# Optimization experiments

Measured on AMD Instinct MI355X. Metric: run time of the kernel, lower is better.

## Reference

```python
import jax, jax.numpy as jnp
import numpy as np

D_MODEL = 1024
NUM_HEADS = 16
HEAD_DIM = D_MODEL // NUM_HEADS
THETA = 10000.0
B, T = 2, 2048


def setup_inputs() -> dict:
    key = jax.random.key(0)
    k1, k2, k3 = jax.random.split(key, 3)
    x = jax.random.normal(k1, (B, T, D_MODEL), dtype=jnp.float32)
    W_qkv = jax.random.normal(k2, (3 * D_MODEL, D_MODEL), dtype=jnp.float32) * 0.02
    W_o = jax.random.normal(k3, (D_MODEL, D_MODEL), dtype=jnp.float32) * 0.02
    return {"x": x, "W_qkv": W_qkv, "W_o": W_o}


def _rope(x, cos, sin):
    # x: [B, h, T, d]; rotate interleaved even/odd pairs
    x_even = x[..., 0::2]
    x_odd = x[..., 1::2]
    out_even = x_even * cos - x_odd * sin
    out_odd = x_even * sin + x_odd * cos
    out = jnp.stack([out_even, out_odd], axis=-1)  # [B,h,T,d/2,2]
    return out.reshape(x.shape)


def reference(x, W_qkv, W_o):
    b, t, dm = x.shape
    # fused QKV projection (bias-free Linear: x @ W.T)
    qkv = jnp.einsum('btd,ed->bte', x, W_qkv)                # [B,T,3*D]
    qkv = qkv.reshape(b, t, 3, NUM_HEADS, HEAD_DIM)
    qkv = jnp.transpose(qkv, (2, 0, 3, 1, 4))                # [3,B,h,T,d]
    q, k, v = qkv[0], qkv[1], qkv[2]

    # RoPE with token_positions = arange(T)
    pos = jnp.arange(t, dtype=jnp.float32)                   # [T]
    inv_freq = THETA ** (-jnp.arange(0, HEAD_DIM, 2, dtype=jnp.float32) / HEAD_DIM)
    ang = pos[:, None] * inv_freq[None, :]                   # [T, d/2]
    cos = jnp.cos(ang)[None, None, :, :]
    sin = jnp.sin(ang)[None, None, :, :]
    q = _rope(q, cos, sin)
    k = _rope(k, cos, sin)

    # causal scaled dot-product attention
    scale = 1.0 / jnp.sqrt(jnp.asarray(HEAD_DIM, dtype=x.dtype))
    scores = jnp.einsum('bhqd,bhkd->bhqk', q, k) * scale     # [B,h,T,T]
    causal = jnp.tril(jnp.ones((t, t), dtype=bool))
    scores = jnp.where(causal[None, None, :, :], scores, -jnp.inf)
    attn = jax.nn.softmax(scores, axis=-1)
    out = jnp.einsum('bhqk,bhkd->bhqd', attn, v)             # [B,h,T,d]
    out = jnp.transpose(out, (0, 2, 1, 3)).reshape(b, t, dm) # [B,T,D]
    return jnp.einsum('btd,ed->bte', out, W_o)
```

## Files before the change

kernel.cpp:

```cpp
#include <hip/hip_runtime.h>
#include <hip/hip_bf16.h>
#include <cstdint>

#define NHEADS 16
#define HDIM 64
#define BB 2
#define TSEQ 2048
#define DM 1024
#define MROWS (BB*TSEQ)

typedef unsigned short u16;
typedef unsigned int u32;
typedef __bf16 bf16x8 __attribute__((ext_vector_type(8)));
typedef float f32x4 __attribute__((ext_vector_type(4)));

#define AS1C(p) ((const __attribute__((address_space(1))) u32*)(p))
#define AS3(p)  ((__attribute__((address_space(3))) u32*)(p))

static __device__ __forceinline__ u16 f2bf(float f) {
  return __builtin_bit_cast(u16, __float2bfloat16(f));
}
static __device__ __forceinline__ float bf2f(u16 u) {
  return __bfloat162float(__builtin_bit_cast(__hip_bfloat16, u));
}
static __device__ __forceinline__ u32 pack2bf(float a, float b) {
  const u32 ua = __builtin_bit_cast(u32, a) + 0x8000u;
  const u32 ub = __builtin_bit_cast(u32, b) + 0x8000u;
  return (ua >> 16) | (ub & 0xFFFF0000u);
}
static __device__ __forceinline__ f32x4 mfma16x16(bf16x8 a, bf16x8 b, f32x4 c) {
  return __builtin_amdgcn_mfma_f32_16x16x32_bf16(a, b, c, 0, 0, 0);
}

#define N4_X   (MROWS * DM / 4)
#define N4_WQ  (3 * DM * DM / 4)
#define N4_WO  (DM * DM / 4)
__global__ __launch_bounds__(256) void cast_all(const float* __restrict__ x,
                                                const float* __restrict__ wq,
                                                const float* __restrict__ wo,
                                                u16* __restrict__ xb,
                                                u16* __restrict__ wqb,
                                                u16* __restrict__ wob) {
  int i = blockIdx.x * 256 + threadIdx.x;
  const int stride = gridDim.x * 256;
  for (; i < N4_X + N4_WQ + N4_WO; i += stride) {
    const float4* src; u16* dst; int j;
    if (i < N4_X)            { src = (const float4*)x;  dst = xb;  j = i; }
    else if (i < N4_X + N4_WQ) { src = (const float4*)wq; dst = wqb; j = i - N4_X; }
    else                     { src = (const float4*)wo; dst = wob; j = i - N4_X - N4_WQ; }
    float4 v = src[j];
    ushort4 o;
    o.x = f2bf(v.x); o.y = f2bf(v.y); o.z = f2bf(v.z); o.w = f2bf(v.w);
    ((ushort4*)dst)[j] = o;
  }
}

template<int WRITE_BF16>
__global__ __launch_bounds__(256, 2) void gemm_bt(const u16* __restrict__ A,
                                                  const u16* __restrict__ Bm,
                                                  float* __restrict__ Cf,
                                                  u16* __restrict__ Cb,
                                                  int M, int N, int K) {
  __shared__ u16 lA[2][128 * 32];
  __shared__ u16 lB[2][128 * 32];
  const int tid = threadIdx.x;
  const int w = tid >> 6, l = tid & 63;
  const int wr = w >> 1, wc = w & 1;
  int bid = blockIdx.y * gridDim.x + blockIdx.x;
  const int cpx = (gridDim.x * gridDim.y) >> 3;
  bid = (bid & 7) * cpx + (bid >> 3);
  const int bx = bid % gridDim.x, by = bid / gridDim.x;
  const int brow = by * 128, bcol = bx * 128;
  const int lr = l & 15, lg = l >> 4;

  const int srow = l >> 2;
  const int scol = (((l & 3) ^ (srow & 3)) * 8);

  auto stage = [&](int buf, int k0) {
#pragma unroll
    for (int is = 0; is < 2; ++is) {
      const int chunk = w * 2 + is;
      const int row = chunk * 16 + srow;
      __builtin_amdgcn_global_load_lds(AS1C(A + (size_t)(brow + row) * K + k0 + scol),
                                       AS3((char*)lA[buf] + chunk * 1024), 16, 0, 0);
      __builtin_amdgcn_global_load_lds(AS1C(Bm + (size_t)(bcol + row) * K + k0 + scol),
                                       AS3((char*)lB[buf] + chunk * 1024), 16, 0, 0);
    }
  };

  f32x4 acc[4][4] = {};
  const int nk = K >> 5;
  stage(0, 0);
  for (int kk = 0; kk < nk; ++kk) {
    const int cur = kk & 1;
    __syncthreads();
    if (kk + 1 < nk) stage(cur ^ 1, (kk + 1) << 5);
    bf16x8 af[4], bfr[4];
#pragma unroll
    for (int m = 0; m < 4; ++m) {
      const int row = wr * 64 + m * 16 + lr;
      const int sl = lg ^ (row & 3);
      af[m] = *(const bf16x8*)(&lA[cur][row * 32 + sl * 8]);
    }
#pragma unroll
    for (int n = 0; n < 4; ++n) {
      const int row = wc * 64 + n * 16 + lr;
      const int sl = lg ^ (row & 3);
      bfr[n] = *(const bf16x8*)(&lB[cur][row * 32 + sl * 8]);
    }
#pragma unroll
    for (int m = 0; m < 4; ++m)
#pragma unroll
      for (int n = 0; n < 4; ++n)
        acc[m][n] = mfma16x16(af[m], bfr[n], acc[m][n]);
  }
#pragma unroll
  for (int m = 0; m < 4; ++m)
#pragma unroll
    for (int n = 0; n < 4; ++n)
#pragma unroll
      for (int r = 0; r < 4; ++r) {
        const int row = brow + wr * 64 + m * 16 + lg * 4 + r;
        const int col = bcol + wc * 64 + n * 16 + lr;
        if constexpr (WRITE_BF16)
          Cb[(size_t)row * N + col] = f2bf(acc[m][n][r]);
        else
          Cf[(size_t)row * N + col] = acc[m][n][r];
      }
}

__global__ __launch_bounds__(256) void rope_reshape(const u16* __restrict__ qkvb,
                                                    u16* __restrict__ qb,
                                                    u16* __restrict__ kb,
                                                    u16* __restrict__ vbT) {
  const int bh = blockIdx.y;
  const int b = bh >> 4, h = bh & 15;
  const int t0 = blockIdx.x * 64;
  const int tid = threadIdx.x;
  const float C = -0.4152410118609203f;
  const float QS = 0.125f * 1.44269504088896341f;

  for (int idx = tid; idx < 64 * 32; idx += 256) {
    const int tl = idx >> 5, p = idx & 31;
    const int t = t0 + tl;
    const size_t base = ((size_t)(b * TSEQ + t)) * 3072 + h * 64 + 2 * p;
    const float qe = bf2f(qkvb[base]), qo = bf2f(qkvb[base + 1]);
    const float ke = bf2f(qkvb[base + 1024]), ko = bf2f(qkvb[base + 1025]);
    const float inv = exp2f((float)p * C);
    const float ang = (float)t * inv;
    float sn, cs;
    sincosf(ang, &sn, &cs);
    const size_t ob = ((size_t)bh * TSEQ + t) * 64 + 2 * p;
    qb[ob]     = f2bf((qe * cs - qo * sn) * QS);
    qb[ob + 1] = f2bf((qe * sn + qo * cs) * QS);
    kb[ob]     = f2bf(ke * cs - ko * sn);
    kb[ob + 1] = f2bf(ke * sn + ko * cs);
  }

  __shared__ u16 lT[64][65];
  for (int idx = tid; idx < 64 * 64; idx += 256) {
    const int tl = idx >> 6, d = idx & 63;
    lT[tl][d] = qkvb[((size_t)(b * TSEQ + t0 + tl)) * 3072 + 2048 + h * 64 + d];
  }
  __syncthreads();
  for (int idx = tid; idx < 64 * 64; idx += 256) {
    const int d = idx >> 6, tl = idx & 63;
    vbT[((size_t)bh * 64 + d) * TSEQ + t0 + tl] = lT[tl][d];
  }
}

__global__ __launch_bounds__(512, 4) void attn_fwd(const u16* __restrict__ qb,
                                                   const u16* __restrict__ kb,
                                                   const u16* __restrict__ vbT,
                                                   u16* __restrict__ ob) {
  __shared__ u16 lK[4][64 * 64];
  __shared__ u16 lV[4][64 * 64];
  __shared__ u16 lP[8][16 * 64];
  const int hw = blockIdx.x;
  const int logical = (hw & 7) * 64 + (hw >> 3);
  const int bh = logical >> 4;
  const int pair = logical & 15;
  const int b = bh >> 4, h = bh & 15;
  const int tid = threadIdx.x;
  const int w = tid >> 6, l = tid & 63;
  const int g = w >> 2, wq = w & 3;
  const int lr = l & 15, lg = l >> 4;
  const int srow8 = l >> 3;
  const int scol = ((l & 7) ^ srow8) * 8;
  const u16* Kb = kb + (size_t)bh * TSEQ * 64;
  const u16* Vb = vbT + (size_t)bh * 64 * TSEQ;
  u16* lPw = lP[w];

  auto stage = [&](int buf, int kt) {
#pragma unroll
    for (int is = 0; is < 2; ++is) {
      const int chunk = wq * 2 + is;
      const int row = chunk * 8 + srow8;
      __builtin_amdgcn_global_load_lds(AS1C(Kb + (size_t)(kt * 64 + row) * 64 + scol),
                                       AS3((char*)lK[buf] + chunk * 1024), 16, 0, 0);
      __builtin_amdgcn_global_load_lds(AS1C(Vb + (size_t)row * TSEQ + kt * 64 + scol),
                                       AS3((char*)lV[buf] + chunk * 1024), 16, 0, 0);
    }
  };

  for (int half = 0; half < 2; ++half) {
    const int qt = half ? (TSEQ / 64 - 1 - pair) : pair;
    const int q0 = qt * 64;

    bf16x8 qf[2];
    {
      const u16* qp = qb + ((size_t)bh * TSEQ + q0 + wq * 16 + lr) * 64 + lg * 8;
      qf[0] = *(const bf16x8*)qp;
      qf[1] = *(const bf16x8*)(qp + 32);
    }

    f32x4 oacc[4] = {};
    float lsum = 0.f;

    const int nt = qt + 1;
    const int nit = (nt + 1) >> 1;
    const int ql = wq * 16 + lr;

    __syncthreads();
    if (g < nt) stage(g * 2, g);
    for (int it = 0; it < nit; ++it) {
      const int cur = it & 1;
      __syncthreads();
      const int ktn = 2 * (it + 1) + g;
      if (ktn < nt) stage(g * 2 + (cur ^ 1), ktn);
      const int kt = 2 * it + g;
      if (kt < nt) {
        const u16* Kc = lK[g * 2 + cur];
        const u16* Vc = lV[g * 2 + cur];

        f32x4 s[4] = {};
        __builtin_amdgcn_s_setprio(1);
#pragma unroll
        for (int n = 0; n < 4; ++n) {
          const int row = n * 16 + lr;
#pragma unroll
          for (int ks = 0; ks < 2; ++ks) {
            const int sl = (ks * 4 + lg) ^ (row & 7);
            bf16x8 kf = *(const bf16x8*)(&Kc[row * 64 + sl * 8]);
            s[n] = mfma16x16(kf, qf[ks], s[n]);
          }
        }
        __builtin_amdgcn_s_setprio(0);

        const bool diag = (kt == qt);
#pragma unroll
        for (int n = 0; n < 4; ++n) {
          float pv[4];
#pragma unroll
          for (int r = 0; r < 4; ++r) {
            float p = __builtin_amdgcn_exp2f(s[n][r]);
            if (diag && (n * 16 + lg * 4 + r > ql)) p = 0.f;
            pv[r] = p;
            lsum += p;
          }
          const u32 w0 = pack2bf(pv[0], pv[1]);
          const u32 w1 = pack2bf(pv[2], pv[3]);
          const int phys = (n * 2 + (lg >> 1)) ^ (lr & 7);
          uint2 pk; pk.x = w0; pk.y = w1;
          *(uint2*)(&lPw[lr * 64 + phys * 8 + (lg & 1) * 4]) = pk;
        }

        bf16x8 pf[2];
#pragma unroll
        for (int ks = 0; ks < 2; ++ks) {
          const int phys = (ks * 4 + lg) ^ (lr & 7);
          pf[ks] = *(const bf16x8*)(&lPw[lr * 64 + phys * 8]);
        }
        __builtin_amdgcn_s_setprio(1);
#pragma unroll
        for (int n = 0; n < 4; ++n) {
          const int row = n * 16 + lr;
#pragma unroll
          for (int ks = 0; ks < 2; ++ks) {
            const int sl = (ks * 4 + lg) ^ (row & 7);
            bf16x8 vf = *(const bf16x8*)(&Vc[row * 64 + sl * 8]);
            oacc[n] = mfma16x16(vf, pf[ks], oacc[n]);
          }
        }
        __builtin_amdgcn_s_setprio(0);
      }
    }

    lsum += __shfl_xor(lsum, 16);
    lsum += __shfl_xor(lsum, 32);

    __syncthreads();
    float* mO = (float*)&lK[0][0];
    float* mL = (float*)&lV[0][0];
    if (g == 1) {
#pragma unroll
      for (int n = 0; n < 4; ++n)
#pragma unroll
        for (int r = 0; r < 4; ++r) {
          const int d = n * 16 + lg * 4 + r;
          mO[wq * 1024 + d * 16 + lr] = oacc[n][r];
        }
      if (lg == 0) mL[wq * 16 + lr] = lsum;
    }
    __syncthreads();
    if (g == 0) {
      const float rl = 1.f / (lsum + mL[wq * 16 + lr]);
      const int q = q0 + wq * 16 + lr;
#pragma unroll
      for (int n = 0; n < 4; ++n) {
        ushort4 ov;
#pragma unroll
        for (int r = 0; r < 4; ++r) {
          const int d = n * 16 + lg * 4 + r;
          const float o = oacc[n][r] + mO[wq * 1024 + d * 16 + lr];
          ((u16*)&ov)[r] = f2bf(o * rl);
        }
        *(ushort4*)(&ob[(size_t)(b * TSEQ + q) * DM + h * 64 + n * 16 + lg * 4]) = ov;
      }
    }
  }
}

extern "C" void kernel_launch(void* const* d_in, const int* in_sizes, int n_in,
                              void* d_out, int out_size, void* d_ws, size_t ws_size,
                              hipStream_t stream) {
  const float* x    = (const float*)d_in[0];
  const float* Wqkv = (const float*)d_in[1];
  const float* Wo   = (const float*)d_in[2];
  float* out = (float*)d_out;

  char* ws = (char*)d_ws;
  u16* xb    = (u16*)ws; ws += (size_t)MROWS * DM * 2;
  u16* wqkvb = (u16*)ws; ws += (size_t)3 * DM * DM * 2;
  u16* wob   = (u16*)ws; ws += (size_t)DM * DM * 2;
  u16* qkvb  = (u16*)ws; ws += (size_t)MROWS * 3 * DM * 2;
  u16* qb    = (u16*)ws; ws += (size_t)BB * NHEADS * TSEQ * HDIM * 2;
  u16* kb    = (u16*)ws; ws += (size_t)BB * NHEADS * TSEQ * HDIM * 2;
  u16* vbT   = (u16*)ws; ws += (size_t)BB * NHEADS * TSEQ * HDIM * 2;
  u16* ob    = (u16*)ws; ws += (size_t)MROWS * DM * 2;

  cast_all<<<2048, 256, 0, stream>>>(x, Wqkv, Wo, xb, wqkvb, wob);

  gemm_bt<1><<<dim3(3 * DM / 128, MROWS / 128), 256, 0, stream>>>(
      xb, wqkvb, nullptr, qkvb, MROWS, 3 * DM, DM);

  rope_reshape<<<dim3(TSEQ / 64, BB * NHEADS), 256, 0, stream>>>(qkvb, qb, kb, vbT);

  attn_fwd<<<512, 512, 0, stream>>>(qb, kb, vbT, ob);

  gemm_bt<0><<<dim3(DM / 128, MROWS / 128), 256, 0, stream>>>(
      ob, wob, out, nullptr, MROWS, DM, DM);
}
```

Measured before the change: 111.5 us.

## Process 128-row query tiles per block to reuse each K/V tile twice

Result: slower. 129.5 us (+16.1%).

```diff
diff --git a/kernel.cpp b/kernel.cpp
--- a/kernel.cpp
+++ b/kernel.cpp
@@ -173,13 +173,13 @@
                                                    const u16* __restrict__ kb,
                                                    const u16* __restrict__ vbT,
                                                    u16* __restrict__ ob) {
-  __shared__ u16 lK[4][64 * 64];
-  __shared__ u16 lV[4][64 * 64];
+  __shared__ u16 lK[2][2][64 * 64];
+  __shared__ u16 lV[2][2][64 * 64];
   __shared__ u16 lP[8][16 * 64];
   const int hw = blockIdx.x;
   const int logical = (hw & 7) * 64 + (hw >> 3);
   const int bh = logical >> 4;
-  const int pair = logical & 15;
+  const int j = 15 - (logical & 15);
   const int b = bh >> 4, h = bh & 15;
   const int tid = threadIdx.x;
   const int w = tid >> 6, l = tid & 63;
@@ -191,128 +191,160 @@
   const u16* Vb = vbT + (size_t)bh * 64 * TSEQ;
   u16* lPw = lP[w];
 
+  const int q0 = j * 128;
+  const int ntiles = 2 * j + 2;
+  const int nit = j + 1;
+  const int dtile = 2 * j + (wq >> 1);
+  const int qa0 = q0 + wq * 32 + lr;
+
+  bf16x8 qf[2][2];
+  {
+    const u16* qp = qb + ((size_t)bh * TSEQ + q0 + wq * 32 + lr) * 64 + lg * 8;
+    qf[0][0] = *(const bf16x8*)qp;
+    qf[0][1] = *(const bf16x8*)(qp + 32);
+    qp += 16 * 64;
+    qf[1][0] = *(const bf16x8*)qp;
+    qf[1][1] = *(const bf16x8*)(qp + 32);
+  }
+
+  f32x4 o0[4] = {}, o1[4] = {};
+  float ls0 = 0.f, ls1 = 0.f;
+
   auto stage = [&](int buf, int kt) {
 #pragma unroll
     for (int is = 0; is < 2; ++is) {
       const int chunk = wq * 2 + is;
       const int row = chunk * 8 + srow8;
       __builtin_amdgcn_global_load_lds(AS1C(Kb + (size_t)(kt * 64 + row) * 64 + scol),
-                                       AS3((char*)lK[buf] + chunk * 1024), 16, 0, 0);
+                                       AS3((char*)lK[g][buf] + chunk * 1024), 16, 0, 0);
       __builtin_amdgcn_global_load_lds(AS1C(Vb + (size_t)row * TSEQ + kt * 64 + scol),
-                                       AS3((char*)lV[buf] + chunk * 1024), 16, 0, 0);
+                                       AS3((char*)lV[g][buf] + chunk * 1024), 16, 0, 0);
     }
   };
 
-  for (int half = 0; half < 2; ++half) {
-    const int qt = half ? (TSEQ / 64 - 1 - pair) : pair;
-    const int q0 = qt * 64;
-
-    bf16x8 qf[2];
-    {
-      const u16* qp = qb + ((size_t)bh * TSEQ + q0 + wq * 16 + lr) * 64 + lg * 8;
-      qf[0] = *(const bf16x8*)qp;
-      qf[1] = *(const bf16x8*)(qp + 32);
-    }
-
-    f32x4 oacc[4] = {};
-    float lsum = 0.f;
-
-    const int nt = qt + 1;
-    const int nit = (nt + 1) >> 1;
-    const int ql = wq * 16 + lr;
-
+  stage(0, g);
+  for (int it = 0; it < nit; ++it) {
+    const int cur = it & 1;
     __syncthreads();
-    if (g < nt) stage(g * 2, g);
-    for (int it = 0; it < nit; ++it) {
-      const int cur = it & 1;
-      __syncthreads();
-      const int ktn = 2 * (it + 1) + g;
-      if (ktn < nt) stage(g * 2 + (cur ^ 1), ktn);
-      const int kt = 2 * it + g;
-      if (kt < nt) {
-        const u16* Kc = lK[g * 2 + cur];
-        const u16* Vc = lV[g * 2 + cur];
-
-        f32x4 s[4] = {};
-        __builtin_amdgcn_s_setprio(1);
-#pragma unroll
-        for (int n = 0; n < 4; ++n) {
-          const int row = n * 16 + lr;
-#pragma unroll
-          for (int ks = 0; ks < 2; ++ks) {
-            const int sl = (ks * 4 + lg) ^ (row & 7);
-            bf16x8 kf = *(const bf16x8*)(&Kc[row * 64 + sl * 8]);
-            s[n] = mfma16x16(kf, qf[ks], s[n]);
-          }
-        }
-        __builtin_amdgcn_s_setprio(0);
-
-        const bool diag = (kt == qt);
-#pragma unroll
-        for (int n = 0; n < 4; ++n) {
-          float pv[4];
-#pragma unroll
-          for (int r = 0; r < 4; ++r) {
-            float p = __builtin_amdgcn_exp2f(s[n][r]);
-            if (diag && (n * 16 + lg * 4 + r > ql)) p = 0.f;
-            pv[r] = p;
-            lsum += p;
-          }
-          const u32 w0 = pack2bf(pv[0], pv[1]);
-          const u32 w1 = pack2bf(pv[2], pv[3]);
-          const int phys = (n * 2 + (lg >> 1)) ^ (lr & 7);
-          uint2 pk; pk.x = w0; pk.y = w1;
-          *(uint2*)(&lPw[lr * 64 + phys * 8 + (lg & 1) * 4]) = pk;
-        }
-
-        bf16x8 pf[2];
+    const int ktn = 2 * (it + 1) + g;
+    if (ktn < ntiles) stage(cur ^ 1, ktn);
+    const int kt = 2 * it + g;
+    if (kt <= dtile) {
+      const u16* Kc = lK[g][cur];
+      const u16* Vc = lV[g][cur];
+
+      f32x4 s0[4] = {}, s1[4] = {};
+      __builtin_amdgcn_s_setprio(1);
+#pragma unroll
+      for (int n = 0; n < 4; ++n) {
+        const int row = n * 16 + lr;
 #pragma unroll
         for (int ks = 0; ks < 2; ++ks) {
-          const int phys = (ks * 4 + lg) ^ (lr & 7);
-          pf[ks] = *(const bf16x8*)(&lPw[lr * 64 + phys * 8]);
-        }
-        __builtin_amdgcn_s_setprio(1);
-#pragma unroll
-        for (int n = 0; n < 4; ++n) {
-          const int row = n * 16 + lr;
-#pragma unroll
-          for (int ks = 0; ks < 2; ++ks) {
-            const int sl = (ks * 4 + lg) ^ (row & 7);
-            bf16x8 vf = *(const bf16x8*)(&Vc[row * 64 + sl * 8]);
-            oacc[n] = mfma16x16(vf, pf[ks], oacc[n]);
-          }
-        }
-        __builtin_amdgcn_s_setprio(0);
-      }
-    }
-
-    lsum += __shfl_xor(lsum, 16);
-    lsum += __shfl_xor(lsum, 32);
-
-    __syncthreads();
-    float* mO = (float*)&lK[0][0];
-    float* mL = (float*)&lV[0][0];
-    if (g == 1) {
+          const int sl = (ks * 4 + lg) ^ (row & 7);
+          bf16x8 kf = *(const bf16x8*)(&Kc[row * 64 + sl * 8]);
+          s0[n] = mfma16x16(kf, qf[0][ks], s0[n]);
+          s1[n] = mfma16x16(kf, qf[1][ks], s1[n]);
+        }
+      }
+      __builtin_amdgcn_s_setprio(0);
+
+      const bool diag = (kt == dtile);
+      const int kvb = kt * 64;
+
+#pragma unroll
+      for (int n = 0; n < 4; ++n) {
+        float pv[4];
+#pragma unroll
+        for (int r = 0; r < 4; ++r) {
+          float p = __builtin_amdgcn_exp2f(s0[n][r]);
+          if (diag && (kvb + n * 16 + lg * 4 + r > qa0)) p = 0.f;
+          pv[r] = p;
+          ls0 += p;
+        }
+        const int phys = (n * 2 + (lg >> 1)) ^ (lr & 7);
+        uint2 pk; pk.x = pack2bf(pv[0], pv[1]); pk.y = pack2bf(pv[2], pv[3]);
+        *(uint2*)(&lPw[lr * 64 + phys * 8 + (lg & 1) * 4]) = pk;
+      }
+      bf16x8 pf0[2];
+#pragma unroll
+      for (int ks = 0; ks < 2; ++ks) {
+        const int phys = (ks * 4 + lg) ^ (lr & 7);
+        pf0[ks] = *(const bf16x8*)(&lPw[lr * 64 + phys * 8]);
+      }
+
+#pragma unroll
+      for (int n = 0; n < 4; ++n) {
+        float pv[4];
+#pragma unroll
+        for (int r = 0; r < 4; ++r) {
+          float p = __builtin_amdgcn_exp2f(s1[n][r]);
+          if (diag && (kvb + n * 16 + lg * 4 + r > qa0 + 16)) p = 0.f;
+          pv[r] = p;
+          ls1 += p;
+        }
+        const int phys = (n * 2 + (lg >> 1)) ^ (lr & 7);
+        uint2 pk; pk.x = pack2bf(pv[0], pv[1]); pk.y = pack2bf(pv[2], pv[3]);
+        *(uint2*)(&lPw[lr * 64 + phys * 8 + (lg & 1) * 4]) = pk;
+      }
+      bf16x8 pf1[2];
+#pragma unroll
+      for (int ks = 0; ks < 2; ++ks) {
+        const int phys = (ks * 4 + lg) ^ (lr & 7);
+        pf1[ks] = *(const bf16x8*)(&lPw[lr * 64 + phys * 8]);
+      }
+
+      __builtin_amdgcn_s_setprio(1);
+#pragma unroll
+      for (int n = 0; n < 4; ++n) {
+        const int row = n * 16 + lr;
+#pragma unroll
+        for (int ks = 0; ks < 2; ++ks) {
+          const int sl = (ks * 4 + lg) ^ (row & 7);
+          bf16x8 vf = *(const bf16x8*)(&Vc[row * 64 + sl * 8]);
+          o0[n] = mfma16x16(vf, pf0[ks], o0[n]);
+          o1[n] = mfma16x16(vf, pf1[ks], o1[n]);
+        }
+      }
+      __builtin_amdgcn_s_setprio(0);
+    }
+  }
+
+  ls0 += __shfl_xor(ls0, 16); ls0 += __shfl_xor(ls0, 32);
+  ls1 += __shfl_xor(ls1, 16); ls1 += __shfl_xor(ls1, 32);
+
+  __syncthreads();
+  float* mO = (float*)&lK[0][0][0];
+  float* mL = (float*)&lV[0][0][0];
+  if (g == 1) {
+#pragma unroll
+    for (int qs = 0; qs < 2; ++qs)
 #pragma unroll
       for (int n = 0; n < 4; ++n)
 #pragma unroll
         for (int r = 0; r < 4; ++r) {
           const int d = n * 16 + lg * 4 + r;
-          mO[wq * 1024 + d * 16 + lr] = oacc[n][r];
-        }
-      if (lg == 0) mL[wq * 16 + lr] = lsum;
-    }
-    __syncthreads();
-    if (g == 0) {
-      const float rl = 1.f / (lsum + mL[wq * 16 + lr]);
-      const int q = q0 + wq * 16 + lr;
+          mO[((wq * 2 + qs) * 64 + d) * 16 + lr] = (qs ? o1[n][r] : o0[n][r]);
+        }
+    if (lg == 0) {
+      mL[(wq * 2 + 0) * 16 + lr] = ls0;
+      mL[(wq * 2 + 1) * 16 + lr] = ls1;
+    }
+  }
+  __syncthreads();
+  if (g == 0) {
+    const float rl0 = 1.f / (ls0 + mL[(wq * 2 + 0) * 16 + lr]);
+    const float rl1 = 1.f / (ls1 + mL[(wq * 2 + 1) * 16 + lr]);
+#pragma unroll
+    for (int qs = 0; qs < 2; ++qs) {
+      const int q = q0 + wq * 32 + qs * 16 + lr;
+      const float rl = qs ? rl1 : rl0;
 #pragma unroll
       for (int n = 0; n < 4; ++n) {
         ushort4 ov;
 #pragma unroll
         for (int r = 0; r < 4; ++r) {
           const int d = n * 16 + lg * 4 + r;
-          const float o = oacc[n][r] + mO[wq * 1024 + d * 16 + lr];
+          const float o = (qs ? o1[n][r] : o0[n][r]) + mO[((wq * 2 + qs) * 64 + d) * 16 + lr];
           ((u16*)&ov)[r] = f2bf(o * rl);
         }
         *(ushort4*)(&ob[(size_t)(b * TSEQ + q) * DM + h * 64 + n * 16 + lg * 4]) = ov;
```

## Load V fragments straight to registers and vectorize RoPE with hardware sincos

Applied to the files above, without the earlier changes.

Result: slower. 145.0 us (+30.0%).

```diff
diff --git a/kernel.cpp b/kernel.cpp
--- a/kernel.cpp
+++ b/kernel.cpp
@@ -139,22 +139,32 @@
   const int tid = threadIdx.x;
   const float C = -0.4152410118609203f;
   const float QS = 0.125f * 1.44269504088896341f;
-
-  for (int idx = tid; idx < 64 * 32; idx += 256) {
-    const int tl = idx >> 5, p = idx & 31;
+  const float R2PI = 0.15915494309189535f;
+
+  for (int idx = tid; idx < 64 * 8; idx += 256) {
+    const int tl = idx >> 3, grp = idx & 7;
     const int t = t0 + tl;
-    const size_t base = ((size_t)(b * TSEQ + t)) * 3072 + h * 64 + 2 * p;
-    const float qe = bf2f(qkvb[base]), qo = bf2f(qkvb[base + 1]);
-    const float ke = bf2f(qkvb[base + 1024]), ko = bf2f(qkvb[base + 1025]);
-    const float inv = exp2f((float)p * C);
-    const float ang = (float)t * inv;
-    float sn, cs;
-    sincosf(ang, &sn, &cs);
-    const size_t ob = ((size_t)bh * TSEQ + t) * 64 + 2 * p;
-    qb[ob]     = f2bf((qe * cs - qo * sn) * QS);
-    qb[ob + 1] = f2bf((qe * sn + qo * cs) * QS);
-    kb[ob]     = f2bf(ke * cs - ko * sn);
-    kb[ob + 1] = f2bf(ke * sn + ko * cs);
+    const size_t base = ((size_t)(b * TSEQ + t)) * 3072 + h * 64 + grp * 8;
+    u16 qv[8], kv8[8], qo[8], ko[8];
+    *(uint4*)qv  = *(const uint4*)(qkvb + base);
+    *(uint4*)kv8 = *(const uint4*)(qkvb + base + 1024);
+#pragma unroll
+    for (int j = 0; j < 4; ++j) {
+      const int p = grp * 4 + j;
+      const float inv = exp2f((float)p * C);
+      const float rev = __builtin_amdgcn_fractf((float)t * inv * R2PI);
+      const float sn = __builtin_amdgcn_sinf(rev);
+      const float cs = __builtin_amdgcn_cosf(rev);
+      const float qe = bf2f(qv[2 * j]), qoo = bf2f(qv[2 * j + 1]);
+      const float ke = bf2f(kv8[2 * j]), koo = bf2f(kv8[2 * j + 1]);
+      qo[2 * j]     = f2bf((qe * cs - qoo * sn) * QS);
+      qo[2 * j + 1] = f2bf((qe * sn + qoo * cs) * QS);
+      ko[2 * j]     = f2bf(ke * cs - koo * sn);
+      ko[2 * j + 1] = f2bf(ke * sn + koo * cs);
+    }
+    const size_t obase = ((size_t)bh * TSEQ + t) * 64 + grp * 8;
+    *(uint4*)(qb + obase) = *(uint4*)qo;
+    *(uint4*)(kb + obase) = *(uint4*)ko;
   }
 
   __shared__ u16 lT[64][65];
@@ -169,12 +179,11 @@
   }
 }
 
-__global__ __launch_bounds__(512, 4) void attn_fwd(const u16* __restrict__ qb,
+__global__ __launch_bounds__(512, 2) void attn_fwd(const u16* __restrict__ qb,
                                                    const u16* __restrict__ kb,
                                                    const u16* __restrict__ vbT,
                                                    u16* __restrict__ ob) {
   __shared__ u16 lK[4][64 * 64];
-  __shared__ u16 lV[4][64 * 64];
   __shared__ u16 lP[8][16 * 64];
   const int hw = blockIdx.x;
   const int logical = (hw & 7) * 64 + (hw >> 3);
@@ -197,14 +206,12 @@
       const int chunk = wq * 2 + is;
       const int row = chunk * 8 + srow8;
       __builtin_amdgcn_global_load_lds(AS1C(Kb + (size_t)(kt * 64 + row) * 64 + scol),
-                                       AS3((char*)lK[buf] + chunk * 1024), 16, 0, 0);
-      __builtin_amdgcn_global_load_lds(AS1C(Vb + (size_t)row * TSEQ + kt * 64 + scol),
-                                       AS3((char*)lV[buf] + chunk * 1024), 16, 0, 0);
+                                       AS3((char*)lK[g * 2 + buf] + chunk * 1024), 16, 0, 0);
     }
   };
 
   for (int half = 0; half < 2; ++half) {
-    const int qt = half ? (TSEQ / 64 - 1 - pair) : pair;
+    const int qt = half ? (31 - pair) : pair;
     const int q0 = qt * 64;
 
     bf16x8 qf[2];
@@ -222,16 +229,23 @@
     const int ql = wq * 16 + lr;
 
     __syncthreads();
-    if (g < nt) stage(g * 2, g);
+    if (g < nt) stage(0, g);
     for (int it = 0; it < nit; ++it) {
       const int cur = it & 1;
       __syncthreads();
       const int ktn = 2 * (it + 1) + g;
-      if (ktn < nt) stage(g * 2 + (cur ^ 1), ktn);
+      if (ktn < nt) stage(cur ^ 1, ktn);
       const int kt = 2 * it + g;
       if (kt < nt) {
         const u16* Kc = lK[g * 2 + cur];
-        const u16* Vc = lV[g * 2 + cur];
+        const int kv0 = kt * 64;
+
+        bf16x8 vf[4][2];
+#pragma unroll
+        for (int n = 0; n < 4; ++n)
+#pragma unroll
+          for (int ks = 0; ks < 2; ++ks)
+            vf[n][ks] = *(const bf16x8*)(Vb + (size_t)(n * 16 + lr) * TSEQ + kv0 + (ks * 4 + lg) * 8);
 
         f32x4 s[4] = {};
         __builtin_amdgcn_s_setprio(1);
@@ -273,15 +287,10 @@
         }
         __builtin_amdgcn_s_setprio(1);
 #pragma unroll
-        for (int n = 0; n < 4; ++n) {
-          const int row = n * 16 + lr;
-#pragma unroll
-          for (int ks = 0; ks < 2; ++ks) {
-            const int sl = (ks * 4 + lg) ^ (row & 7);
-            bf16x8 vf = *(const bf16x8*)(&Vc[row * 64 + sl * 8]);
-            oacc[n] = mfma16x16(vf, pf[ks], oacc[n]);
-          }
-        }
+        for (int n = 0; n < 4; ++n)
+#pragma unroll
+          for (int ks = 0; ks < 2; ++ks)
+            oacc[n] = mfma16x16(vf[n][ks], pf[ks], oacc[n]);
         __builtin_amdgcn_s_setprio(0);
       }
     }
@@ -291,7 +300,7 @@
 
     __syncthreads();
     float* mO = (float*)&lK[0][0];
-    float* mL = (float*)&lV[0][0];
+    float* mL = (float*)&lP[0][0];
     if (g == 1) {
 #pragma unroll
       for (int n = 0; n < 4; ++n)
```
